# Performance work log

Measured on AMD Instinct MI355X. Metric: run time of the kernel, lower is better.

Reference implementation:

```python
import jax, jax.numpy as jnp
import numpy as np
import math

NUM_HEADS = 8
KEY_DIM = 32
VALUE_DIM = 32
ERF = 3                      # local window (erf x erf), N = 1 + ERF*ERF key/query positions
PAD = (ERF - 1) // 2
STRIDE = 2
OUT_CH = 256


def unfold_2d(x, k, p, s):
    """Mirror of F.unfold -> (B, k*k, C, Ho, Wo), window index row-major (kh, kw)."""
    B, C, H, W = x.shape
    xp = jnp.pad(x, ((0, 0), (0, 0), (p, p), (p, p)))
    Ho = (H + 2 * p - k) // s + 1
    Wo = (W + 2 * p - k) // s + 1
    pats = [xp[:, :, i:i + s * (Ho - 1) + 1:s, j:j + s * (Wo - 1) + 1:s]
            for i in range(k) for j in range(k)]
    return jnp.stack(pats, axis=1)


def fold_2d(pats, out_hw, k, p, s):
    """Mirror of F.fold (overlap-add inverse of unfold_2d)."""
    B, kk, C, Ho, Wo = pats.shape
    H, W = out_hw
    out = jnp.zeros((B, C, H + 2 * p, W + 2 * p), pats.dtype)
    idx = 0
    for i in range(k):
        for j in range(k):
            out = out.at[:, :, i:i + s * (Ho - 1) + 1:s, j:j + s * (Wo - 1) + 1:s].add(pats[:, idx])
            idx += 1
    return out[:, :, p:p + H, p:p + W]


def setup_inputs() -> dict:
    key = jax.random.key(0)
    ks = jax.random.split(key, 10)
    B = 2
    d = {
        "top_feat": jax.random.normal(ks[0], (B, OUT_CH, 64, 64), jnp.float32),
        "bot_feat": jax.random.normal(ks[1], (B, OUT_CH, 128, 128), jnp.float32),
    }
    qkv_names = ["W_top_key", "W_top_query", "W_top_value", "W_bot_key", "W_bot_query", "W_bot_value"]
    for n, kk in zip(qkv_names, ks[2:8]):
        out_dim = NUM_HEADS * (KEY_DIM if ("key" in n or "query" in n) else VALUE_DIM)
        d[n] = 0.01 * jax.random.normal(kk, (out_dim, OUT_CH), jnp.float32)  # 1x1 conv, no bias
    d["W_top_fuse"] = 0.01 * jax.random.normal(ks[8], (OUT_CH, NUM_HEADS * VALUE_DIM), jnp.float32)
    d["W_bot_fuse"] = 0.01 * jax.random.normal(ks[9], (OUT_CH, NUM_HEADS * VALUE_DIM), jnp.float32)
    return d


def _forward(top_feat, bot_feat, W_top_key, W_top_query, W_top_value,
             W_bot_key, W_bot_query, W_bot_value, W_top_fuse, W_bot_fuse):
    B, _, H, W = top_feat.shape
    Hb, Wb = bot_feat.shape[2], bot_feat.shape[3]

    def proj(x, Wm, dim):  # 1x1 conv then split heads -> (B, h, dim, H', W')
        y = jnp.einsum('oc,bchw->bohw', Wm, x)
        return y.reshape(B, NUM_HEADS, dim, x.shape[2], x.shape[3])

    def unfold_heads(x):  # (B, h, d, Hb, Wb) -> (B, h, e*e, d, H, W)
        d = x.shape[2]
        u = unfold_2d(x.reshape(B * NUM_HEADS, d, Hb, Wb), ERF, PAD, STRIDE)
        return u.reshape(B, NUM_HEADS, ERF * ERF, d, u.shape[3], u.shape[4])

    tK = proj(top_feat, W_top_key, KEY_DIM)[:, :, None]      # (B, h, 1, kd, H, W)
    tQ = proj(top_feat, W_top_query, KEY_DIM)[:, :, None]
    tV = proj(top_feat, W_top_value, VALUE_DIM)[:, :, None]
    bK = unfold_heads(proj(bot_feat, W_bot_key, KEY_DIM))    # (B, h, e*e, kd, H, W)
    bQ = unfold_heads(proj(bot_feat, W_bot_query, KEY_DIM))
    bV = unfold_heads(proj(bot_feat, W_bot_value, VALUE_DIM))

    key_ = jnp.concatenate([tK, bK], axis=2)   # (B, h, N, kd, H, W), N = 1 + e*e
    query = jnp.concatenate([tQ, bQ], axis=2)
    value = jnp.concatenate([tV, bV], axis=2)

    # weight[b,n,k,q,h,w] = <key_k, query_q> / sqrt(kd)   (NOTE: no softmax in original)
    weight = jnp.einsum('bnkdhw,bnqdhw->bnkqhw', key_, query) / math.sqrt(KEY_DIM)
    # out[b,n,q,v,h,w] = sum_k weight[...] * value_k
    out = jnp.einsum('bnkqhw,bnkvhw->bnqvhw', weight, value)  # (B, h, N, vd, H, W)

    top_ret = out[:, :, 0].reshape(B, NUM_HEADS * VALUE_DIM, H, W)
    bot_pat = out[:, :, 1:].reshape(B * NUM_HEADS, ERF * ERF, VALUE_DIM, H, W)
    bot_ret = fold_2d(bot_pat, (Hb, Wb), ERF, PAD, STRIDE).reshape(B, NUM_HEADS * VALUE_DIM, Hb, Wb)

    top_out = jnp.einsum('oc,bchw->bohw', W_top_fuse, top_ret)
    bot_out = jnp.einsum('oc,bchw->bohw', W_bot_fuse, bot_ret)
    return top_out, bot_out


def reference(top_feat, bot_feat, W_top_key, W_top_query, W_top_value,
              W_bot_key, W_bot_query, W_bot_value, W_top_fuse, W_bot_fuse):
    return _forward(top_feat, bot_feat, W_top_key, W_top_query, W_top_value,
                    W_bot_key, W_bot_query, W_bot_value, W_top_fuse, W_bot_fuse)
```

## Files before the change

kernel.cpp:

```cpp
#include <hip/hip_runtime.h>
#include <hip/hip_bf16.h>
#include <math.h>


typedef __attribute__((ext_vector_type(8))) short  bh8;
typedef __attribute__((ext_vector_type(4))) short  bh4;
typedef __attribute__((ext_vector_type(4))) float  f32x4;
typedef unsigned short u16;

static __device__ __forceinline__ u16 f2b(float x) {
    __hip_bfloat16 h = __float2bfloat16(x);
    return __builtin_bit_cast(u16, h);
}
static __device__ __forceinline__ float b2f(u16 u) {
    unsigned v = ((unsigned)u) << 16;
    return __builtin_bit_cast(float, v);
}

static __device__ __forceinline__ void gload16(const u16* g, u16* l) {
    __builtin_amdgcn_global_load_lds(
        (const __attribute__((address_space(1))) unsigned int*)g,
        (__attribute__((address_space(3))) unsigned int*)l, 16, 0, 0);
}

__global__ __launch_bounds__(256) void k_prep(
    const float* w0, const float* w1, const float* w2, const float* w3,
    const float* w4, const float* w5, const float* w6, const float* w7,
    const float* __restrict__ top_feat, const float* __restrict__ bot_feat,
    u16* __restrict__ Wb, u16* __restrict__ topT, u16* __restrict__ botT)
{
    __shared__ float T[64][65];
    const int bid = blockIdx.x;
    const int t   = threadIdx.x;

    if (bid < 512) {
        const int mat = bid >> 6;
        const float* src;
        switch (mat) {
            case 0: src = w0; break; case 1: src = w1; break;
            case 2: src = w2; break; case 3: src = w3; break;
            case 4: src = w4; break; case 5: src = w5; break;
            case 6: src = w6; break; default: src = w7; break;
        }
        int i = ((bid & 63) * 256 + t) * 4;
        float4 v = *(const float4*)&src[i];
        u16 tmp[4] = { f2b(v.x), f2b(v.y), f2b(v.z), f2b(v.w) };
        *(uint2*)&Wb[(size_t)mat * 65536 + i] = *(uint2*)tmp;
        return;
    }

    const float* in; u16* outp; int S, b, s0, c0;
    if (bid < 1024) {
        int i = bid - 512;
        b = i >> 8; int rem = i & 255;
        s0 = (rem & 63) * 64; c0 = (rem >> 6) * 64;
        in = top_feat; outp = topT; S = 4096;
    } else {
        int i = bid - 1024;
        b = i >> 10; int rem = i & 1023;
        s0 = (rem & 255) * 64; c0 = (rem >> 8) * 64;
        in = bot_feat; outp = botT; S = 16384;
    }
    in   += (size_t)b * 256 * S;
    outp += (size_t)b * S * 256;
    {
        int cc = t >> 4, f4 = t & 15;
        #pragma unroll
        for (int rep = 0; rep < 4; ++rep) {
            int c = cc + rep * 16;
            float4 v = *(const float4*)&in[(size_t)(c0 + c) * S + s0 + f4 * 4];
            T[c][f4*4+0] = v.x; T[c][f4*4+1] = v.y;
            T[c][f4*4+2] = v.z; T[c][f4*4+3] = v.w;
        }
    }
    __syncthreads();
    {
        int sr = t >> 3, u = t & 7;
        #pragma unroll
        for (int rep = 0; rep < 2; ++rep) {
            int s = sr + rep * 32;
            u16 tmp[8];
            #pragma unroll
            for (int e = 0; e < 8; ++e) tmp[e] = f2b(T[u*8+e][s]);
            *(uint4*)&outp[(size_t)(s0 + s) * 256 + c0 + u * 8] = *(uint4*)tmp;
        }
    }
}

#define GEMM_STAGE(bufi, kk) do {                                             \
        _Pragma("unroll")                                                     \
        for (int it = 0; it < 2; ++it) {                                      \
            int lin = it * 256 + t;                                           \
            int row = lin >> 3, c = lin & 7;                                  \
            int cs = c ^ (row & 7);                                           \
            gload16(&A[(size_t)(m0 + row) * 256 + (kk) + cs * 8],             \
                    &AT[bufi][lin * 8]);                                      \
        }                                                                     \
        _Pragma("unroll")                                                     \
        for (int it = 0; it < 8; ++it) {                                      \
            int lin = it * 256 + t;                                           \
            int row = lin >> 3, c = lin & 7;                                  \
            int cs = c ^ (row & 7);                                           \
            gload16(&B[(size_t)(n0 + row) * 256 + (kk) + cs * 8],             \
                    &BT[bufi][lin * 8]);                                      \
        }                                                                     \
    } while (0)

#define GEMM_MAIN()                                                           \
    GEMM_STAGE(0, 0);                                                         \
    int cur = 0;                                                              \
    for (int kt = 0; kt < 4; ++kt) {                                          \
        __syncthreads();                                                      \
        if (kt < 3) GEMM_STAGE(cur ^ 1, (kt + 1) * 64);                       \
        _Pragma("unroll")                                                     \
        for (int ks = 0; ks < 2; ++ks) {                                      \
            bh8 af[4], bf[4];                                                 \
            _Pragma("unroll")                                                 \
            for (int mi = 0; mi < 4; ++mi) {                                  \
                int row = mi * 16 + l16;                                      \
                int pc = (ks * 4 + grp) ^ (row & 7);                          \
                af[mi] = *(const bh8*)&AT[cur][row * 64 + pc * 8];            \
            }                                                                 \
            _Pragma("unroll")                                                 \
            for (int ni = 0; ni < 4; ++ni) {                                  \
                int row = w * 64 + ni * 16 + l16;                             \
                int pc = (ks * 4 + grp) ^ (row & 7);                          \
                bf[ni] = *(const bh8*)&BT[cur][row * 64 + pc * 8];            \
            }                                                                 \
            _Pragma("unroll")                                                 \
            for (int mi = 0; mi < 4; ++mi)                                    \
                _Pragma("unroll")                                             \
                for (int ni = 0; ni < 4; ++ni)                                \
                    acc[mi][ni] = __builtin_amdgcn_mfma_f32_16x16x32_bf16(    \
                        af[mi], bf[ni], acc[mi][ni], 0, 0, 0);                \
        }                                                                     \
        cur ^= 1;                                                             \
    }

__global__ __launch_bounds__(256) void k_proj(
    const u16* __restrict__ topT, const u16* __restrict__ botT,
    const u16* __restrict__ Wb,
    u16* __restrict__ tK, u16* __restrict__ bK, size_t TOPU, size_t BOTU)
{
    const int yb    = blockIdx.y;
    const bool istop = yb < 128;
    const u16* A = istop ? topT : botT;
    const u16* B = istop ? Wb : (Wb + 3 * 65536);
    u16* Yp      = istop ? tK : bK;
    const size_t arrsz = istop ? TOPU : BOTU;
    const int m0 = (istop ? yb : (yb - 128)) * 64;
    const int n0 = blockIdx.x * 256;
    const int t  = threadIdx.x;
    const int w  = t >> 6, wl = t & 63, l16 = wl & 15, grp = wl >> 4;

    __shared__ __align__(16) u16 AT[2][64 * 64];
    __shared__ __align__(16) u16 BT[2][256 * 64];

    f32x4 acc[4][4];
    #pragma unroll
    for (int i = 0; i < 4; ++i)
        #pragma unroll
        for (int j = 0; j < 4; ++j) acc[i][j] = (f32x4){0.f, 0.f, 0.f, 0.f};

    GEMM_MAIN();

    #pragma unroll
    for (int mi = 0; mi < 4; ++mi)
        #pragma unroll
        for (int ni = 0; ni < 4; ++ni)
            #pragma unroll
            for (int r = 0; r < 4; ++r) {
                int m = m0 + mi*16 + grp*4 + r;
                int n = n0 + w*64 + ni*16 + l16;
                Yp[(size_t)(n >> 8) * arrsz + (size_t)m * 256 + (n & 255)]
                    = f2b(acc[mi][ni][r]);
            }
}

__global__ __launch_bounds__(256) void k_fuse(
    const u16* __restrict__ Wb, const u16* __restrict__ tRet,
    const u16* __restrict__ botRet, float* __restrict__ top_out,
    float* __restrict__ bot_out)
{
    const int bid = blockIdx.x;
    const u16* A; const u16* B; float* Yf; int lgS, n0, m0;
    if (bid < 128) {
        A = Wb + 6 * 65536; B = tRet; Yf = top_out; lgS = 12;
        n0 = (bid & 31) * 256; m0 = (bid >> 5) * 64;
    } else {
        int i = bid - 128;
        A = Wb + 7 * 65536; B = botRet; Yf = bot_out; lgS = 14;
        n0 = (i & 127) * 256; m0 = (i >> 7) * 64;
    }
    const int t  = threadIdx.x;
    const int w  = t >> 6, wl = t & 63, l16 = wl & 15, grp = wl >> 4;

    __shared__ __align__(16) u16 AT[2][64 * 64];
    __shared__ __align__(16) u16 BT[2][256 * 64];

    f32x4 acc[4][4];
    #pragma unroll
    for (int i = 0; i < 4; ++i)
        #pragma unroll
        for (int j = 0; j < 4; ++j) acc[i][j] = (f32x4){0.f, 0.f, 0.f, 0.f};

    GEMM_MAIN();

    #pragma unroll
    for (int mi = 0; mi < 4; ++mi)
        #pragma unroll
        for (int ni = 0; ni < 4; ++ni)
            #pragma unroll
            for (int r = 0; r < 4; ++r) {
                int m = m0 + mi*16 + grp*4 + r;
                int n = n0 + w*64 + ni*16 + l16;
                int bb = n >> lgS, s = n & ((1 << lgS) - 1);
                Yf[(((size_t)bb * 256 + m) << lgS) + s] = acc[mi][ni][r];
            }
}

__global__ __launch_bounds__(256) void k_attn(
    const u16* __restrict__ tK, const u16* __restrict__ tQ, const u16* __restrict__ tV,
    const u16* __restrict__ bK, const u16* __restrict__ bQ, const u16* __restrict__ bV,
    u16* __restrict__ tRet, u16* __restrict__ pat)
{
    const int pix = blockIdx.x;
    const int b   = blockIdx.y;
    const int w   = threadIdx.x >> 6;
    const int wl  = threadIdx.x & 63;
    const int l16 = wl & 15, grp = wl >> 4;
    const int y = pix >> 6, x = pix & 63;

    __shared__ u16 Ssm[4][16][24];
    __shared__ __align__(16) u16 Vsm[4][2][16][16];

    const int p = l16;
    bool pvalid = false; int bpix = 0; const bool istop = (p == 0);
    if (p == 0) pvalid = true;
    else if (p < 10) {
        int pm = p - 1; int i = (pm * 11) >> 5; int j = pm - 3 * i;
        int by = 2 * y + i - 1, bx = 2 * x + j - 1;
        pvalid = ((unsigned)by < 128u) && ((unsigned)bx < 128u);
        bpix = by * 128 + bx;
    }
    const size_t topRow = ((size_t)b * 4096  + pix)  * 256;
    const size_t botRow = ((size_t)b * 16384 + bpix) * 256;
    const float scale = 0.17677669529663687f;

    #pragma unroll
    for (int hi = 0; hi < 2; ++hi) {
        const int h = w + hi * 4;
        const size_t off = (istop ? topRow : botRow) + h * 32 + grp * 8;
        bh8 aQ = {}, aK = {}, vV = {};
        if (pvalid) {
            if (istop) {
                aQ = *(const bh8*)(tQ + off);
                aK = *(const bh8*)(tK + off);
                vV = *(const bh8*)(tV + off);
            } else {
                aQ = *(const bh8*)(bQ + off);
                aK = *(const bh8*)(bK + off);
                vV = *(const bh8*)(bV + off);
            }
        }
        *(bh8*)&Vsm[w][grp >> 1][p][(grp & 1) * 8] = vV;

        f32x4 z = {0.f, 0.f, 0.f, 0.f};
        f32x4 sC = __builtin_amdgcn_mfma_f32_16x16x32_bf16(aQ, aK, z, 0, 0, 0);
        #pragma unroll
        for (int r = 0; r < 4; ++r)
            Ssm[w][grp * 4 + r][l16] = f2b(sC[r] * scale);

        bh8 aS = {};
        *(bh4*)&aS = *(const bh4*)&Ssm[w][l16][grp * 4];

        bh8 bv0 = {}, bv1 = {};
        #pragma unroll
        for (int j = 0; j < 4; ++j) {
            bv0[j] = (short)Vsm[w][0][grp * 4 + j][l16];
            bv1[j] = (short)Vsm[w][1][grp * 4 + j][l16];
        }
        f32x4 oc0 = __builtin_amdgcn_mfma_f32_16x16x32_bf16(aS, bv0, z, 0, 0, 0);
        f32x4 oc1 = __builtin_amdgcn_mfma_f32_16x16x32_bf16(aS, bv1, z, 0, 0, 0);

        if (grp == 0) {
            size_t o = topRow + (size_t)h * 32;
            tRet[o + l16]      = f2b(oc0[0]);
            tRet[o + 16 + l16] = f2b(oc1[0]);
        }
        #pragma unroll
        for (int r = 0; r < 4; ++r) {
            int q = grp * 4 + r;
            if (q >= 1 && q <= 9) {
                size_t base = ((((size_t)b * 8 + h) * 9 + (q - 1)) * 4096 + pix) * 32;
                pat[base + l16]      = f2b(oc0[r]);
                pat[base + 16 + l16] = f2b(oc1[r]);
            }
        }
    }
}

__global__ __launch_bounds__(256) void k_fold(
    const u16* __restrict__ pat, u16* __restrict__ botRet)
{
    int tid = blockIdx.x * 256 + threadIdx.x;
    int vchunk = tid & 3;
    int ri = tid >> 2;
    int b = ri >> 17;
    int bpix = (ri >> 3) & 16383;
    int h = ri & 7;
    int by = bpix >> 7, bx = bpix & 127;
    int v0 = vchunk * 8;

    float acc[8];
    #pragma unroll
    for (int e = 0; e < 8; ++e) acc[e] = 0.f;

    for (int iy = 0; iy < 3; ++iy) {
        int ty = by + 1 - iy;
        if (ty & 1) continue;
        int yy = ty >> 1;
        if ((unsigned)yy >= 64u) continue;
        for (int jx = 0; jx < 3; ++jx) {
            int tx = bx + 1 - jx;
            if (tx & 1) continue;
            int xx = tx >> 1;
            if ((unsigned)xx >= 64u) continue;
            int q = iy * 3 + jx;
            size_t addr = ((((size_t)b * 8 + h) * 9 + q) * 4096 + (yy * 64 + xx)) * 32 + v0;
            uint4 pv = *(const uint4*)&pat[addr];
            const u16* pp = (const u16*)&pv;
            #pragma unroll
            for (int e = 0; e < 8; ++e) acc[e] += b2f(pp[e]);
        }
    }
    u16 tmp[8];
    #pragma unroll
    for (int e = 0; e < 8; ++e) tmp[e] = f2b(acc[e]);
    *(uint4*)&botRet[((size_t)b * 16384 + bpix) * 256 + h * 32 + v0] = *(uint4*)tmp;
}

extern "C" void kernel_launch(void* const* d_in, const int* in_sizes, int n_in,
                              void* d_out, int out_size, void* d_ws, size_t ws_size,
                              hipStream_t stream) {
    const float* top_feat = (const float*)d_in[0];
    const float* bot_feat = (const float*)d_in[1];

    float* out     = (float*)d_out;
    float* top_out = out;
    float* bot_out = out + (size_t)2 * 256 * 4096;

    const size_t TOPU = (size_t)2 * 4096  * 256;
    const size_t BOTU = (size_t)2 * 16384 * 256;
    char* p = (char*)d_ws;
    u16* Wb     = (u16*)p;  p += (size_t)8 * 65536 * 2;
    u16* topT   = (u16*)p;  p += TOPU * 2;
    u16* botT   = (u16*)p;  p += BOTU * 2;
    u16* tK     = (u16*)p;  p += TOPU * 2;
    u16* tQ     = (u16*)p;  p += TOPU * 2;
    u16* tV     = (u16*)p;  p += TOPU * 2;
    u16* bK     = (u16*)p;  p += BOTU * 2;
    u16* bQ     = (u16*)p;  p += BOTU * 2;
    u16* bV     = (u16*)p;  p += BOTU * 2;
    u16* tRet   = (u16*)p;  p += TOPU * 2;
    u16* pat    = (u16*)p;  p += (size_t)2*8*9*4096*32*2;
    u16* botRet = (u16*)p;  p += BOTU * 2;

    dim3 blk(256);

    k_prep<<<dim3(3072), blk, 0, stream>>>(
        (const float*)d_in[2], (const float*)d_in[3], (const float*)d_in[4],
        (const float*)d_in[5], (const float*)d_in[6], (const float*)d_in[7],
        (const float*)d_in[8], (const float*)d_in[9],
        top_feat, bot_feat, Wb, topT, botT);

    k_proj<<<dim3(3, 640), blk, 0, stream>>>(topT, botT, Wb, tK, bK, TOPU, BOTU);

    k_attn<<<dim3(4096, 2), blk, 0, stream>>>(tK, tQ, tV, bK, bQ, bV, tRet, pat);

    k_fold<<<dim3(4096), blk, 0, stream>>>(pat, botRet);

    k_fuse<<<dim3(640), blk, 0, stream>>>(Wb, tRet, botRet, top_out, bot_out);
}
```

Measured before the change: 102.5 us.

## Fuse feature transpose and bf16 conversion into projection GEMM A-tile load

The separate prep pass that transposed the fp32 feature maps into bf16 channel-last buffers is removed. The projection GEMM now reads fp32 features directly from NCHW, converts them in registers, and writes swizzled bf16 tiles into LDS, prefetching the next k-tile through registers. Weight conversion moves to its own small kernel. This avoids writing and re-reading the transposed intermediates, but each projection block now re-reads fp32 activations once per N-tile (three times) and uses plain register loads instead of direct-to-LDS loads.

```diff
diff --git a/kernel.cpp b/kernel.cpp
--- a/kernel.cpp
+++ b/kernel.cpp
@@ -23,68 +23,133 @@
         (__attribute__((address_space(3))) unsigned int*)l, 16, 0, 0);
 }
 
-__global__ __launch_bounds__(256) void k_prep(
+__global__ __launch_bounds__(256) void k_cvt_w(
     const float* w0, const float* w1, const float* w2, const float* w3,
     const float* w4, const float* w5, const float* w6, const float* w7,
+    u16* __restrict__ Wb)
+{
+    const float* srcs[8] = {w0,w1,w2,w3,w4,w5,w6,w7};
+    const float* src = srcs[blockIdx.y];
+    int i = (blockIdx.x * 256 + threadIdx.x) * 4;
+    float4 v = *(const float4*)&src[i];
+    u16 tmp[4] = { f2b(v.x), f2b(v.y), f2b(v.z), f2b(v.w) };
+    *(uint2*)&Wb[(size_t)blockIdx.y * 65536 + i] = *(uint2*)tmp;
+}
+
+__global__ __launch_bounds__(256) void k_proj(
     const float* __restrict__ top_feat, const float* __restrict__ bot_feat,
-    u16* __restrict__ Wb, u16* __restrict__ topT, u16* __restrict__ botT)
+    const u16* __restrict__ Wb,
+    u16* __restrict__ tK, u16* __restrict__ bK, size_t TOPU, size_t BOTU)
 {
-    __shared__ float T[64][65];
-    const int bid = blockIdx.x;
-    const int t   = threadIdx.x;
-
-    if (bid < 512) {
-        const int mat = bid >> 6;
-        const float* src;
-        switch (mat) {
-            case 0: src = w0; break; case 1: src = w1; break;
-            case 2: src = w2; break; case 3: src = w3; break;
-            case 4: src = w4; break; case 5: src = w5; break;
-            case 6: src = w6; break; default: src = w7; break;
-        }
-        int i = ((bid & 63) * 256 + t) * 4;
-        float4 v = *(const float4*)&src[i];
-        u16 tmp[4] = { f2b(v.x), f2b(v.y), f2b(v.z), f2b(v.w) };
-        *(uint2*)&Wb[(size_t)mat * 65536 + i] = *(uint2*)tmp;
-        return;
-    }
-
-    const float* in; u16* outp; int S, b, s0, c0;
-    if (bid < 1024) {
-        int i = bid - 512;
-        b = i >> 8; int rem = i & 255;
-        s0 = (rem & 63) * 64; c0 = (rem >> 6) * 64;
-        in = top_feat; outp = topT; S = 4096;
-    } else {
-        int i = bid - 1024;
-        b = i >> 10; int rem = i & 1023;
-        s0 = (rem & 255) * 64; c0 = (rem >> 8) * 64;
-        in = bot_feat; outp = botT; S = 16384;
-    }
-    in   += (size_t)b * 256 * S;
-    outp += (size_t)b * S * 256;
-    {
-        int cc = t >> 4, f4 = t & 15;
-        #pragma unroll
-        for (int rep = 0; rep < 4; ++rep) {
-            int c = cc + rep * 16;
-            float4 v = *(const float4*)&in[(size_t)(c0 + c) * S + s0 + f4 * 4];
-            T[c][f4*4+0] = v.x; T[c][f4*4+1] = v.y;
-            T[c][f4*4+2] = v.z; T[c][f4*4+3] = v.w;
-        }
-    }
-    __syncthreads();
-    {
-        int sr = t >> 3, u = t & 7;
-        #pragma unroll
-        for (int rep = 0; rep < 2; ++rep) {
-            int s = sr + rep * 32;
-            u16 tmp[8];
-            #pragma unroll
-            for (int e = 0; e < 8; ++e) tmp[e] = f2b(T[u*8+e][s]);
-            *(uint4*)&outp[(size_t)(s0 + s) * 256 + c0 + u * 8] = *(uint4*)tmp;
-        }
-    }
+    const int yb    = blockIdx.y;
+    const bool istop = yb < 128;
+    const float* feat = istop ? top_feat : bot_feat;
+    const u16* Bw   = istop ? Wb : (Wb + 3 * 65536);
+    u16* Yp         = istop ? tK : bK;
+    const size_t arrsz = istop ? TOPU : BOTU;
+    const int S     = istop ? 4096 : 16384;
+    const int m0g   = (istop ? yb : (yb - 128)) * 64;
+    const int b     = istop ? (m0g >> 12) : (m0g >> 14);
+    const int pix0  = m0g & (S - 1);
+    const float* Xb = feat + (size_t)b * 256 * S;
+    const int n0 = blockIdx.x * 256;
+    const int t  = threadIdx.x;
+    const int w  = t >> 6, wl = t & 63, l16 = wl & 15, grp = wl >> 4;
+    const int apix = t & 63;
+    const int aq   = t >> 6;
+
+    __shared__ __align__(16) u16 AT[2][64 * 64];
+    __shared__ __align__(16) u16 BT[2][256 * 64];
+
+    float rA[2][8];
+
+#define PROJ_A_LOAD(kk) do {                                                  \
+        _Pragma("unroll")                                                     \
+        for (int cc = 0; cc < 2; ++cc)                                        \
+            _Pragma("unroll")                                                 \
+            for (int e = 0; e < 8; ++e)                                       \
+                rA[cc][e] = Xb[(size_t)((kk) + (2*aq + cc)*8 + e) * S         \
+                               + pix0 + apix];                                \
+    } while (0)
+
+#define PROJ_A_WRITE(bufi) do {                                               \
+        _Pragma("unroll")                                                     \
+        for (int cc = 0; cc < 2; ++cc) {                                      \
+            int cg = 2*aq + cc, slot = cg ^ (apix & 7);                       \
+            u16 tmp[8];                                                       \
+            _Pragma("unroll")                                                 \
+            for (int e = 0; e < 8; ++e) tmp[e] = f2b(rA[cc][e]);              \
+            *(uint4*)&AT[bufi][apix * 64 + slot * 8] = *(uint4*)tmp;          \
+        }                                                                     \
+    } while (0)
+
+#define PROJ_STAGE_B(bufi, kk) do {                                           \
+        _Pragma("unroll")                                                     \
+        for (int it = 0; it < 8; ++it) {                                      \
+            int lin = it * 256 + t;                                           \
+            int row = lin >> 3, c = lin & 7;                                  \
+            int cs = c ^ (row & 7);                                           \
+            gload16(&Bw[(size_t)(n0 + row) * 256 + (kk) + cs * 8],            \
+                    &BT[bufi][lin * 8]);                                      \
+        }                                                                     \
+    } while (0)
+
+    f32x4 acc[4][4];
+    #pragma unroll
+    for (int i = 0; i < 4; ++i)
+        #pragma unroll
+        for (int j = 0; j < 4; ++j) acc[i][j] = (f32x4){0.f, 0.f, 0.f, 0.f};
+
+    PROJ_A_LOAD(0);
+    PROJ_STAGE_B(0, 0);
+    PROJ_A_WRITE(0);
+    int cur = 0;
+    for (int kt = 0; kt < 4; ++kt) {
+        __syncthreads();
+        if (kt < 3) {
+            PROJ_A_LOAD((kt + 1) * 64);
+            PROJ_STAGE_B(cur ^ 1, (kt + 1) * 64);
+        }
+        #pragma unroll
+        for (int ks = 0; ks < 2; ++ks) {
+            bh8 af[4], bf[4];
+            #pragma unroll
+            for (int mi = 0; mi < 4; ++mi) {
+                int row = mi * 16 + l16;
+                int pc = (ks * 4 + grp) ^ (row & 7);
+                af[mi] = *(const bh8*)&AT[cur][row * 64 + pc * 8];
+            }
+            #pragma unroll
+            for (int ni = 0; ni < 4; ++ni) {
+                int row = w * 64 + ni * 16 + l16;
+                int pc = (ks * 4 + grp) ^ (row & 7);
+                bf[ni] = *(const bh8*)&BT[cur][row * 64 + pc * 8];
+            }
+            #pragma unroll
+            for (int mi = 0; mi < 4; ++mi)
+                #pragma unroll
+                for (int ni = 0; ni < 4; ++ni)
+                    acc[mi][ni] = __builtin_amdgcn_mfma_f32_16x16x32_bf16(
+                        af[mi], bf[ni], acc[mi][ni], 0, 0, 0);
+        }
+        if (kt < 3) PROJ_A_WRITE(cur ^ 1);
+        cur ^= 1;
+    }
+#undef PROJ_A_LOAD
+#undef PROJ_A_WRITE
+#undef PROJ_STAGE_B
+
+    #pragma unroll
+    for (int mi = 0; mi < 4; ++mi)
+        #pragma unroll
+        for (int ni = 0; ni < 4; ++ni)
+            #pragma unroll
+            for (int r = 0; r < 4; ++r) {
+                int m = m0g + mi*16 + grp*4 + r;
+                int n = n0 + w*64 + ni*16 + l16;
+                Yp[(size_t)(n >> 8) * arrsz + (size_t)m * 256 + (n & 255)]
+                    = f2b(acc[mi][ni][r]);
+            }
 }
 
 #define GEMM_STAGE(bufi, kk) do {                                             \
@@ -137,46 +202,6 @@
         cur ^= 1;                                                             \
     }
 
-__global__ __launch_bounds__(256) void k_proj(
-    const u16* __restrict__ topT, const u16* __restrict__ botT,
-    const u16* __restrict__ Wb,
-    u16* __restrict__ tK, u16* __restrict__ bK, size_t TOPU, size_t BOTU)
-{
-    const int yb    = blockIdx.y;
-    const bool istop = yb < 128;
-    const u16* A = istop ? topT : botT;
-    const u16* B = istop ? Wb : (Wb + 3 * 65536);
-    u16* Yp      = istop ? tK : bK;
-    const size_t arrsz = istop ? TOPU : BOTU;
-    const int m0 = (istop ? yb : (yb - 128)) * 64;
-    const int n0 = blockIdx.x * 256;
-    const int t  = threadIdx.x;
-    const int w  = t >> 6, wl = t & 63, l16 = wl & 15, grp = wl >> 4;
-
-    __shared__ __align__(16) u16 AT[2][64 * 64];
-    __shared__ __align__(16) u16 BT[2][256 * 64];
-
-    f32x4 acc[4][4];
-    #pragma unroll
-    for (int i = 0; i < 4; ++i)
-        #pragma unroll
-        for (int j = 0; j < 4; ++j) acc[i][j] = (f32x4){0.f, 0.f, 0.f, 0.f};
-
-    GEMM_MAIN();
-
-    #pragma unroll
-    for (int mi = 0; mi < 4; ++mi)
-        #pragma unroll
-        for (int ni = 0; ni < 4; ++ni)
-            #pragma unroll
-            for (int r = 0; r < 4; ++r) {
-                int m = m0 + mi*16 + grp*4 + r;
-                int n = n0 + w*64 + ni*16 + l16;
-                Yp[(size_t)(n >> 8) * arrsz + (size_t)m * 256 + (n & 255)]
-                    = f2b(acc[mi][ni][r]);
-            }
-}
-
 __global__ __launch_bounds__(256) void k_fuse(
     const u16* __restrict__ Wb, const u16* __restrict__ tRet,
     const u16* __restrict__ botRet, float* __restrict__ top_out,
@@ -354,8 +379,6 @@
     const size_t BOTU = (size_t)2 * 16384 * 256;
     char* p = (char*)d_ws;
     u16* Wb     = (u16*)p;  p += (size_t)8 * 65536 * 2;
-    u16* topT   = (u16*)p;  p += TOPU * 2;
-    u16* botT   = (u16*)p;  p += BOTU * 2;
     u16* tK     = (u16*)p;  p += TOPU * 2;
     u16* tQ     = (u16*)p;  p += TOPU * 2;
     u16* tV     = (u16*)p;  p += TOPU * 2;
@@ -368,13 +391,13 @@
 
     dim3 blk(256);
 
-    k_prep<<<dim3(3072), blk, 0, stream>>>(
+    k_cvt_w<<<dim3(64, 8), blk, 0, stream>>>(
         (const float*)d_in[2], (const float*)d_in[3], (const float*)d_in[4],
         (const float*)d_in[5], (const float*)d_in[6], (const float*)d_in[7],
-        (const float*)d_in[8], (const float*)d_in[9],
-        top_feat, bot_feat, Wb, topT, botT);
-
-    k_proj<<<dim3(3, 640), blk, 0, stream>>>(topT, botT, Wb, tK, bK, TOPU, BOTU);
+        (const float*)d_in[8], (const float*)d_in[9], Wb);
+
+    k_proj<<<dim3(3, 640), blk, 0, stream>>>(top_feat, bot_feat, Wb,
+                                             tK, bK, TOPU, BOTU);
 
     k_attn<<<dim3(4096, 2), blk, 0, stream>>>(tK, tQ, tV, bK, bQ, bV, tRet, pat);
 
```

New measurement: 102.3 us. Within noise of the previous version (-0.1%).
